# Performance work log

Measured on AMD Instinct MI355X. Metric: run time of the kernel, lower is better.

The kernel has to match this reference:

```python
import jax, jax.numpy as jnp
import numpy as np

B, T, F, UNITS, OUT_STEPS = 512, 128, 64, 1024, 32


def setup_inputs() -> dict:
    key = jax.random.key(0)
    k0, k1, k2, k3 = jax.random.split(key, 4)
    return {
        "inputs": jax.random.normal(k0, (B, T, F), jnp.float32),
        "Wk": jax.random.normal(k1, (F, 4 * UNITS), jnp.float32) * 0.02,   # input kernel (i,f,c,o)
        "Wr": jax.random.normal(k2, (UNITS, 4 * UNITS), jnp.float32) * 0.02,  # recurrent kernel
        "b": jnp.zeros((4 * UNITS,), jnp.float32),
        "Wd": jax.random.normal(k3, (UNITS, F), jnp.float32) * 0.02,  # output Dense
        "bd": jnp.zeros((F,), jnp.float32),
        "out_steps": OUT_STEPS,
    }


def _lstm_cell(h, c, x, Wk, Wr, b):
    # Keras LSTMCell: z packed as (i, f, g, o); sigmoid gates, tanh cell.
    z = x @ Wk + h @ Wr + b
    i, f, g, o = jnp.split(z, 4, axis=-1)
    c = jax.nn.sigmoid(f) * c + jax.nn.sigmoid(i) * jnp.tanh(g)
    h = jax.nn.sigmoid(o) * jnp.tanh(c)
    return h, c


def reference(inputs, Wk, Wr, b, Wd, bd, out_steps):
    Bn = inputs.shape[0]
    units = Wr.shape[0]
    h0 = jnp.zeros((Bn, units), inputs.dtype)
    c0 = jnp.zeros((Bn, units), inputs.dtype)

    # warmup: run LSTM over the input window, keep final state
    def warm(carry, x_t):
        h, c = carry
        h, c = _lstm_cell(h, c, x_t, Wk, Wr, b)
        return (h, c), None

    (h, c), _ = jax.lax.scan(warm, (h0, c0), jnp.swapaxes(inputs, 0, 1))
    pred0 = h @ Wd + bd  # first-step prediction [B, F]

    def dec(carry, _):
        pred, h, c = carry
        h, c = _lstm_cell(h, c, pred, Wk, Wr, b)
        pred = h @ Wd + bd
        return (pred, h, c), pred

    _, rest = jax.lax.scan(dec, (pred0, h, c), None, length=out_steps - 1)
    preds = jnp.concatenate([pred0[None], rest], axis=0)  # [out_steps, B, F]
    return jnp.transpose(preds, (1, 0, 2))  # [B, out_steps, F]
```

## Files before the change

### kernel.cpp

```cpp
#include <hip/hip_runtime.h>
#include <math.h>

#define BATCH 512
#define TT    128
#define FF    64
#define UU    1024
#define ZZ    4096
#define OS    32
#define KTOT  1088
#define NCH   17
#define CROW  72
#define ABASE 0
#define WBASE (64 * CROW)
#define CBUF  (192 * CROW)

typedef _Float16 f16x8 __attribute__((ext_vector_type(8)));
typedef float f32x16 __attribute__((ext_vector_type(16)));

__device__ __forceinline__ float sigf(float x) { return 1.0f / (1.0f + expf(-x)); }

__global__ __launch_bounds__(256) void wconv(
    const float* __restrict__ Wk, const float* __restrict__ Wr,
    _Float16* __restrict__ WT)
{
    __shared__ float T[32][129];
    const int k0 = blockIdx.x * 32;
    const int n0 = blockIdx.y * 128;
    const int u0 = n0 >> 2;
    const int t = threadIdx.x;
    #pragma unroll
    for (int i = 0; i < 16; ++i) {
        int idx = t + i * 256;
        int u = idx & 31, k = (idx >> 5) & 31, g = idx >> 10;
        int krow = k0 + k;
        int col = g * UU + u0 + u;
        float wv = (krow < FF) ? Wk[(size_t)krow * ZZ + col]
                               : Wr[(size_t)(krow - FF) * ZZ + col];
        T[k][u * 4 + g] = wv;
    }
    __syncthreads();
    #pragma unroll
    for (int i = 0; i < 16; ++i) {
        int idx = t + i * 256;
        int k = idx & 31, np = idx >> 5;
        WT[(size_t)(n0 + np) * KTOT + k0 + k] = (_Float16)T[k][np];
    }
}

__global__ __launch_bounds__(256) void init_k(
    uint4* __restrict__ zbase, const float* __restrict__ x0,
    _Float16* __restrict__ xF)
{
    const int b = blockIdx.x, t = threadIdx.x;
    if (b < 768) {
        zbase[(size_t)b * 256 + t] = make_uint4(0u, 0u, 0u, 0u);
    } else {
        int e = (b - 768) * 256 + t;
        int bb = e >> 6, f = e & 63;
        xF[e] = (_Float16)x0[(size_t)bb * (TT * FF) + f];
    }
}

__global__ __launch_bounds__(512, 2) void lstm_cell_mfma(
    const _Float16* __restrict__ xF,
    const _Float16* __restrict__ hF,
    _Float16* __restrict__ hFo,
    float* __restrict__ c,
    const _Float16* __restrict__ WT,
    const float* __restrict__ bias,
    const float* __restrict__ xnext, _Float16* __restrict__ xnF)
{
    __shared__ __align__(16) char smem[2 * CBUF * 2];
    _Float16* lds = (_Float16*)smem;
    float* z = (float*)smem;

    const int t = threadIdx.x;
    const int lane = t & 63;
    const int w  = t >> 6;
    const int mw = w >> 2;
    const int nw = w & 3;
    const int n0 = blockIdx.x * 128;
    const int r0 = blockIdx.y * 64;
    const int u0 = n0 >> 2;
    const int l31 = lane & 31;

    const int srow = t >> 3;
    const int sseg = t & 7;
    const _Float16* aAx = xF + (size_t)(r0 + srow) * FF + sseg * 8;
    const _Float16* aAh = hF + (size_t)(r0 + srow) * UU + sseg * 8;
    const _Float16* aW0 = WT + (size_t)(n0 + srow) * KTOT + sseg * 8;
    const _Float16* aW1 = WT + (size_t)(n0 + 64 + srow) * KTOT + sseg * 8;
    const int wA  = ABASE + srow * CROW + sseg * 8;
    const int wW0 = WBASE + srow * CROW + sseg * 8;
    const int wW1 = WBASE + (64 + srow) * CROW + sseg * 8;

    uint4 sA[2], sW0[2], sW1[2];

    const int fra = (mw * 32 + l31) * CROW + (lane >> 5) * 8;
    const int frw = WBASE + (nw * 32 + l31) * CROW + (lane >> 5) * 8;

    f32x16 acc;
    #pragma unroll
    for (int i = 0; i < 16; ++i) acc[i] = 0.f;

#define LOADC(ch)                                                              \
    {                                                                          \
        const int _s = (ch) & 1;                                               \
        sA[_s]  = ((ch) == 0) ? *(const uint4*)aAx                             \
                              : *(const uint4*)(aAh + ((ch) - 1) * 64);        \
        sW0[_s] = *(const uint4*)(aW0 + (ch) * 64);                            \
        sW1[_s] = *(const uint4*)(aW1 + (ch) * 64);                            \
    }
#define WRITEC(ch)                                                             \
    {                                                                          \
        const int _s = (ch) & 1;                                               \
        _Float16* _b = lds + _s * CBUF;                                        \
        *(uint4*)(_b + wA)  = sA[_s];                                          \
        *(uint4*)(_b + wW0) = sW0[_s];                                         \
        *(uint4*)(_b + wW1) = sW1[_s];                                         \
    }

    LOADC(0)
    LOADC(1)
    WRITEC(0)

    #pragma unroll
    for (int ch = 0; ch < NCH; ++ch) {
        if (ch + 2 < NCH) LOADC(ch + 2)
        __builtin_amdgcn_s_waitcnt(0xC07F);
        __builtin_amdgcn_s_barrier();
        if (ch + 1 < NCH) WRITEC(ch + 1)
        const _Float16* b = lds + (ch & 1) * CBUF;
        #pragma unroll
        for (int s = 0; s < 4; ++s) {
            f16x8 af = *(const f16x8*)(b + fra + s * 16);
            f16x8 wf = *(const f16x8*)(b + frw + s * 16);
            acc = __builtin_amdgcn_mfma_f32_32x32x16_f16(af, wf, acc, 0, 0, 0);
        }
    }
#undef LOADC
#undef WRITEC

    __syncthreads();

    {
        const int nloc = nw * 32 + l31;
        const int gs = (nloc & 3) * 33 + (nloc >> 2);
        const int rbase = mw * 32 + 4 * (lane >> 5);
        #pragma unroll
        for (int r = 0; r < 16; ++r) {
            int m = rbase + (r & 3) + 8 * (r >> 2);
            z[m * 132 + gs] = acc[r];
        }
    }
    __syncthreads();

    {
        const int ul = t & 31;
        const int uu = u0 + ul;
        const float bi = bias[uu], bfr = bias[UU + uu];
        const float bg = bias[2 * UU + uu], bo = bias[3 * UU + uu];
        #pragma unroll
        for (int rep = 0; rep < 4; ++rep) {
            int m = (t >> 5) * 4 + rep;
            float zi = z[m * 132 + ul];
            float zf = z[m * 132 + 33 + ul];
            float zg = z[m * 132 + 66 + ul];
            float zo = z[m * 132 + 99 + ul];
            size_t idx = (size_t)(r0 + m) * UU + uu;
            float cn = sigf(zf + bfr) * c[idx] + sigf(zi + bi) * tanhf(zg + bg);
            c[idx] = cn;
            hFo[idx] = (_Float16)(sigf(zo + bo) * tanhf(cn));
        }
    }

    if (xnext != nullptr && t < 128) {
        int e = (blockIdx.x + 32 * blockIdx.y) * 128 + t;
        int bb = e >> 6, f = e & 63;
        xnF[e] = (_Float16)xnext[(size_t)bb * (TT * FF) + f];
    }
}

__global__ __launch_bounds__(256) void dense_out(
    const _Float16* __restrict__ hF,
    const float* __restrict__ Wd, const float* __restrict__ bd,
    _Float16* __restrict__ pF, float* __restrict__ outp)
{
    __shared__ float red[4][64];
    const int t = threadIdx.x, f = t & 63, ks = t >> 6, bb = blockIdx.x;
    const f16x8* hr = (const f16x8*)(hF + (size_t)bb * UU + ks * 256);
    const float* wp = Wd + (size_t)(ks * 256) * FF + f;
    float s = 0.f;
    #pragma unroll 4
    for (int v = 0; v < 32; ++v) {
        f16x8 a = hr[v];
        #pragma unroll
        for (int j = 0; j < 8; ++j)
            s += (float)a[j] * wp[(size_t)(v * 8 + j) * FF];
    }
    red[ks][f] = s;
    __syncthreads();
    if (ks == 0) {
        float vv = red[0][f] + red[1][f] + red[2][f] + red[3][f] + bd[f];
        outp[(size_t)bb * (OS * FF) + f] = vv;
        pF[bb * FF + f] = (_Float16)vv;
    }
}

extern "C" void kernel_launch(void* const* d_in, const int* in_sizes, int n_in,
                              void* d_out, int out_size, void* d_ws, size_t ws_size,
                              hipStream_t stream) {
    const float* inputs = (const float*)d_in[0];
    const float* Wk     = (const float*)d_in[1];
    const float* Wr     = (const float*)d_in[2];
    const float* bias   = (const float*)d_in[3];
    const float* Wd     = (const float*)d_in[4];
    const float* bd     = (const float*)d_in[5];
    float* out = (float*)d_out;

    char* ws = (char*)d_ws;
    _Float16* hF0 = (_Float16*)(ws);
    float*    cb  = (float*)(ws + 1048576);
    _Float16* hF1 = (_Float16*)(ws + 3145728);
    _Float16* WT  = (_Float16*)(ws + 4194304);
    _Float16* x0F = (_Float16*)(ws + 13107200);
    _Float16* x1F = (_Float16*)(ws + 13172736);
    _Float16* prF = (_Float16*)(ws + 13238272);

    wconv<<<dim3(34, 32), 256, 0, stream>>>(Wk, Wr, WT);
    init_k<<<896, 256, 0, stream>>>((uint4*)ws, inputs, x0F);

    dim3 cgrid(32, 8);
    _Float16 *hc = hF0, *hn = hF1;

    for (int t = 0; t < TT; ++t) {
        const _Float16* xF = (t & 1) ? x1F : x0F;
        _Float16* xnF = (t & 1) ? x0F : x1F;
        const float* xnext = (t < TT - 1) ? (inputs + (size_t)(t + 1) * FF) : nullptr;
        lstm_cell_mfma<<<cgrid, 512, 0, stream>>>(xF, hc, hn, cb, WT, bias, xnext, xnF);
        _Float16* tp = hc; hc = hn; hn = tp;
    }

    dense_out<<<BATCH, 256, 0, stream>>>(hc, Wd, bd, prF, out);

    for (int s = 1; s < OS; ++s) {
        lstm_cell_mfma<<<cgrid, 512, 0, stream>>>(prF, hc, hn, cb, WT, bias, nullptr, nullptr);
        _Float16* tp = hc; hc = hn; hn = tp;
        dense_out<<<BATCH, 256, 0, stream>>>(hc, Wd, bd, prF, out + (size_t)s * FF);
    }
}
```

Measured before the change: 2.757 ms.

## Pre-swizzle weights into MFMA fragment order and load B operands directly to registers

```diff
diff --git a/kernel.cpp b/kernel.cpp
--- a/kernel.cpp
+++ b/kernel.cpp
@@ -10,9 +10,8 @@
 #define KTOT  1088
 #define NCH   17
 #define CROW  72
-#define ABASE 0
-#define WBASE (64 * CROW)
-#define CBUF  (192 * CROW)
+#define CBUF  (64 * CROW)
+#define NKB   68
 
 typedef _Float16 f16x8 __attribute__((ext_vector_type(8)));
 typedef float f32x16 __attribute__((ext_vector_type(16)));
@@ -43,7 +42,11 @@
     for (int i = 0; i < 16; ++i) {
         int idx = t + i * 256;
         int k = idx & 31, np = idx >> 5;
-        WT[(size_t)(n0 + np) * KTOT + k0 + k] = (_Float16)T[k][np];
+        int r = n0 + np;
+        int kk = k0 + k;
+        size_t o = ((size_t)(r >> 5) * NKB + (kk >> 4)) * 512
+                 + (size_t)((((kk >> 3) & 1) * 32 + (r & 31)) * 8 + (kk & 7));
+        WT[o] = (_Float16)T[k][np];
     }
 }
 
@@ -70,7 +73,7 @@
     const float* __restrict__ bias,
     const float* __restrict__ xnext, _Float16* __restrict__ xnF)
 {
-    __shared__ __align__(16) char smem[2 * CBUF * 2];
+    __shared__ __align__(16) char smem[64 * 132 * 4];
     _Float16* lds = (_Float16*)smem;
     float* z = (float*)smem;
 
@@ -88,58 +91,57 @@
     const int sseg = t & 7;
     const _Float16* aAx = xF + (size_t)(r0 + srow) * FF + sseg * 8;
     const _Float16* aAh = hF + (size_t)(r0 + srow) * UU + sseg * 8;
-    const _Float16* aW0 = WT + (size_t)(n0 + srow) * KTOT + sseg * 8;
-    const _Float16* aW1 = WT + (size_t)(n0 + 64 + srow) * KTOT + sseg * 8;
-    const int wA  = ABASE + srow * CROW + sseg * 8;
-    const int wW0 = WBASE + srow * CROW + sseg * 8;
-    const int wW1 = WBASE + (64 + srow) * CROW + sseg * 8;
-
-    uint4 sA[2], sW0[2], sW1[2];
+    const int wA = srow * CROW + sseg * 8;
+    uint4 sA[2];
+
+    const _Float16* pW = WT + ((size_t)(blockIdx.x * 4 + nw) * NKB) * 512 + lane * 8;
 
     const int fra = (mw * 32 + l31) * CROW + (lane >> 5) * 8;
-    const int frw = WBASE + (nw * 32 + l31) * CROW + (lane >> 5) * 8;
 
     f32x16 acc;
     #pragma unroll
     for (int i = 0; i < 16; ++i) acc[i] = 0.f;
 
-#define LOADC(ch)                                                              \
+    f16x8 wf[3][4];
+
+#define LOADA(ch)                                                              \
     {                                                                          \
-        const int _s = (ch) & 1;                                               \
-        sA[_s]  = ((ch) == 0) ? *(const uint4*)aAx                             \
-                              : *(const uint4*)(aAh + ((ch) - 1) * 64);        \
-        sW0[_s] = *(const uint4*)(aW0 + (ch) * 64);                            \
-        sW1[_s] = *(const uint4*)(aW1 + (ch) * 64);                            \
-    }
-#define WRITEC(ch)                                                             \
+        sA[(ch) & 1] = ((ch) == 0) ? *(const uint4*)aAx                        \
+                                   : *(const uint4*)(aAh + ((ch) - 1) * 64);   \
+    }
+#define LOADW(ch)                                                              \
     {                                                                          \
-        const int _s = (ch) & 1;                                               \
-        _Float16* _b = lds + _s * CBUF;                                        \
-        *(uint4*)(_b + wA)  = sA[_s];                                          \
-        *(uint4*)(_b + wW0) = sW0[_s];                                         \
-        *(uint4*)(_b + wW1) = sW1[_s];                                         \
-    }
-
-    LOADC(0)
-    LOADC(1)
-    WRITEC(0)
+        _Pragma("unroll")                                                      \
+        for (int s = 0; s < 4; ++s)                                            \
+            wf[(ch) % 3][s] = *(const f16x8*)(pW + ((ch) * 4 + s) * 512);      \
+    }
+#define WRITEA(ch)                                                             \
+    {                                                                          \
+        *(uint4*)(lds + ((ch) & 1) * CBUF + wA) = sA[(ch) & 1];                \
+    }
+
+    LOADA(0)
+    LOADW(0)
+    LOADA(1)
+    LOADW(1)
+    WRITEA(0)
 
     #pragma unroll
     for (int ch = 0; ch < NCH; ++ch) {
-        if (ch + 2 < NCH) LOADC(ch + 2)
+        if (ch + 2 < NCH) { LOADA(ch + 2) LOADW(ch + 2) }
         __builtin_amdgcn_s_waitcnt(0xC07F);
         __builtin_amdgcn_s_barrier();
-        if (ch + 1 < NCH) WRITEC(ch + 1)
+        if (ch + 1 < NCH) WRITEA(ch + 1)
         const _Float16* b = lds + (ch & 1) * CBUF;
         #pragma unroll
         for (int s = 0; s < 4; ++s) {
             f16x8 af = *(const f16x8*)(b + fra + s * 16);
-            f16x8 wf = *(const f16x8*)(b + frw + s * 16);
-            acc = __builtin_amdgcn_mfma_f32_32x32x16_f16(af, wf, acc, 0, 0, 0);
+            acc = __builtin_amdgcn_mfma_f32_32x32x16_f16(af, wf[ch % 3][s], acc, 0, 0, 0);
         }
     }
-#undef LOADC
-#undef WRITEC
+#undef LOADA
+#undef LOADW
+#undef WRITEA
 
     __syncthreads();
 
```

Result: faster. 2.696 ms (-2.2%).
